# Kernel tuning notes

Measured on AMD Instinct MI355X. Metric: run time of the kernel, lower is better.

Reference implementation:

```python
import jax, jax.numpy as jnp
import numpy as np

WINDOW_SIZE = 7
C1 = 0.01 ** 2
C2 = 0.03 ** 2


def _gaussian_window(ws: int) -> jnp.ndarray:
    sigma = ws / 6.0
    coords = jnp.arange(ws, dtype=jnp.float32) - ws // 2
    g = jnp.exp(-coords ** 2 / (2 * sigma ** 2))
    g = g / g.sum()
    k3 = g[:, None, None] * g[None, :, None] * g[None, None, :]
    k3 = k3 / k3.sum()
    return k3.reshape(1, 1, ws, ws, ws)  # OIDHW


def _conv3d_same(x, w):
    pad = WINDOW_SIZE // 2
    return jax.lax.conv_general_dilated(
        x, w, window_strides=(1, 1, 1),
        padding=[(pad, pad)] * 3,
        dimension_numbers=('NCDHW', 'OIDHW', 'NCDHW'))


def setup_inputs() -> dict:
    key = jax.random.key(0)
    k1, k2 = jax.random.split(key)
    shape = (2, 1, 160, 160, 160)
    predicted = jax.random.uniform(k1, shape, dtype=jnp.float32)
    target = jax.random.uniform(k2, shape, dtype=jnp.float32)
    return {"predicted": predicted, "target": target}


def reference(predicted, target):
    window = _gaussian_window(WINDOW_SIZE)
    mu1 = _conv3d_same(predicted, window)
    mu2 = _conv3d_same(target, window)
    mu1_sq = mu1 ** 2
    mu2_sq = mu2 ** 2
    mu1_mu2 = mu1 * mu2
    sigma1_sq = _conv3d_same(predicted ** 2, window) - mu1_sq
    sigma2_sq = _conv3d_same(target ** 2, window) - mu2_sq
    sigma12 = _conv3d_same(predicted * target, window) - mu1_mu2
    ssim_map = ((2 * mu1_mu2 + C1) * (2 * sigma12 + C2)) / (
        (mu1_sq + mu2_sq + C1) * (sigma1_sq + sigma2_sq + C2))
    return 1.0 - ssim_map.mean()
```

## Files before the change

kernel.cpp:

```cpp
#include <hip/hip_runtime.h>
#include <math.h>

#define DD 160
#define HH 160
#define WW 160
#define NB 2
#define NEL (NB*DD*HH*WW)

#define XT 32
#define YT 16
#define ZC 16
#define NTHR 256
#define NZCH (DD/ZC)
#define GX (WW/XT)
#define GY (HH/YT)
#define NBLK (GX*GY*NB*NZCH)
#define NPART NBLK

#define HR 22
#define NJOB (HR*8)
#define NJOBW 44
#define CP 35

typedef float v2f __attribute__((ext_vector_type(2)));

struct G7 { float g[7]; };

__global__ __launch_bounds__(NTHR, 4) void ssim_fused(
        const float* __restrict__ p, const float* __restrict__ t,
        float* __restrict__ partial, G7 gw) {
    const int tid = threadIdx.x;
    const int tx  = tid & 31;
    const int tyo = tid >> 5;

    const int flat = blockIdx.x;
    const int w = (flat & 7) * (NBLK / 8) + (flat >> 3);
    const int bx = w % GX;
    const int by = (w / GX) % GY;
    const int bz = w / (GX * GY);

    const int x0 = bx * XT;
    const int y0 = by * YT;
    const int n  = bz / NZCH;
    const int zs = (bz % NZCH) * ZC;
    const int send = zs + ZC + 3;

    __shared__ float4 c4[2][HR][CP];

    v2f r01[2][6], r23[2][6];
#pragma unroll
    for (int yo = 0; yo < 2; ++yo)
#pragma unroll
        for (int j = 0; j < 6; ++j) {
            r01[yo][j] = (v2f)(0.f);
            r23[yo][j] = (v2f)(0.f);
        }

    const float C1v = 1e-4f, C2v = 9e-4f;
    float ssum = 0.f;
    const int hw = HH * WW;
    const float* pv = p + (size_t)n * DD * hw;
    const float* tv = t + (size_t)n * DD * hw;

    const int lane = tid & 63, wv = tid >> 6;
    const int j = wv * NJOBW + lane;
    const bool jok = lane < NJOBW;
    const int br  = j >> 3;
    const int bxg = j & 7;
    const int bgy = y0 + br - 3;
    const bool browok = jok && (unsigned)bgy < (unsigned)HH;
    const int cbase = x0 + 4 * bxg - 4;
    const int pcr = tx + (tx >> 3);
    bool qok[3];
#pragma unroll
    for (int q = 0; q < 3; ++q)
        qok[q] = browok && (unsigned)(cbase + 4 * q) < (unsigned)WW;

    const float* prow = pv + (size_t)(zs - 3) * hw + bgy * WW;
    const float* trow = tv + (size_t)(zs - 3) * hw + bgy * WW;

    float4 pfa[3], pfb[3];
    auto prefetch = [&](int sx) {
#pragma unroll
        for (int q = 0; q < 3; ++q) {
            pfa[q] = make_float4(0.f, 0.f, 0.f, 0.f);
            pfb[q] = make_float4(0.f, 0.f, 0.f, 0.f);
        }
        if (sx >= 0 && sx < DD && sx < send) {
#pragma unroll
            for (int q = 0; q < 3; ++q) {
                if (qok[q]) {
                    pfa[q] = *(const float4*)(prow + cbase + 4 * q);
                    pfb[q] = *(const float4*)(trow + cbase + 4 * q);
                }
            }
        }
    };

    auto do_B = [&](int par) {
        if (jok) {
            v2f s01[4], s23[4];
#pragma unroll
            for (int e = 0; e < 4; ++e) { s01[e] = (v2f)(0.f); s23[e] = (v2f)(0.f); }
#pragma unroll
            for (int q = 0; q < 3; ++q) {
                const float af[4] = {pfa[q].x, pfa[q].y, pfa[q].z, pfa[q].w};
                const float bf[4] = {pfb[q].x, pfb[q].y, pfb[q].z, pfb[q].w};
#pragma unroll
                for (int jj = 0; jj < 4; ++jj) {
                    const int i = 4 * q + jj;
                    v2f pt; pt[0] = af[jj]; pt[1] = bf[jj];
                    v2f ud; ud[0] = af[jj] + bf[jj]; ud[1] = af[jj] - bf[jj];
                    v2f qu = ud * ud;
#pragma unroll
                    for (int e = 0; e < 4; ++e) {
                        const int k = i - e - 1;
                        if (k >= 0 && k < 7) {
                            s01[e] = gw.g[k] * pt + s01[e];
                            s23[e] = gw.g[k] * qu + s23[e];
                        }
                    }
                }
            }
#pragma unroll
            for (int e = 0; e < 4; ++e) {
                int c = 4 * bxg + e;
                c4[par][br][c + (c >> 3)] =
                    make_float4(s01[e][0], s01[e][1], s23[e][0], s23[e][1]);
            }
        }
    };

    prefetch(zs - 3);
    do_B((zs - 3) & 1);
    prow += hw; trow += hw;
    prefetch(zs - 2);

    for (int s = zs - 3; s < send; ++s) {
        __syncthreads();

        if (s + 1 < send) do_B((s + 1) & 1);

        prow += hw; trow += hw;
        prefetch(s + 2);

        v2f m01[2], m23[2];
#pragma unroll
        for (int yo = 0; yo < 2; ++yo) {
            m01[yo] = (v2f)(0.f);
            m23[yo] = (v2f)(0.f);
        }
#pragma unroll
        for (int r8 = 0; r8 < 8; ++r8) {
            float4 v = c4[s & 1][2 * tyo + r8][pcr];
            v2f v01; v01[0] = v.x; v01[1] = v.y;
            v2f v23; v23[0] = v.z; v23[1] = v.w;
            if (r8 < 7) {
                float w2 = gw.g[r8];
                m01[0] = w2 * v01 + m01[0];
                m23[0] = w2 * v23 + m23[0];
            }
            if (r8 > 0) {
                float w2 = gw.g[r8 - 1];
                m01[1] = w2 * v01 + m01[1];
                m23[1] = w2 * v23 + m23[1];
            }
        }

#pragma unroll
        for (int yo = 0; yo < 2; ++yo) {
            v2f v01 = m01[yo], v23 = m23[yo];
            v2f cons01 = gw.g[6] * v01 + r01[yo][0];
            v2f cons23 = gw.g[6] * v23 + r23[yo][0];
#pragma unroll
            for (int jj = 0; jj < 5; ++jj) {
                r01[yo][jj] = gw.g[5 - jj] * v01 + r01[yo][jj + 1];
                r23[yo][jj] = gw.g[5 - jj] * v23 + r23[yo][jj + 1];
            }
            r01[yo][5] = gw.g[0] * v01;
            r23[yo][5] = gw.g[0] * v23;

            if (s >= zs + 3) {
                float mu1 = cons01[0], mu2 = cons01[1];
                float Eu  = cons23[0], Ew  = cons23[1];
                float mu12 = mu1 * mu2, mu1sq = mu1 * mu1, mu2sq = mu2 * mu2;
                float sumsq = 0.5f  * (Eu + Ew) - mu1sq - mu2sq;
                float s12   = 0.25f * (Eu - Ew) - mu12;
                float num = (2.f * mu12 + C1v) * (2.f * s12 + C2v);
                float den = (mu1sq + mu2sq + C1v) * (sumsq + C2v);
                ssum += num * __builtin_amdgcn_rcpf(den);
            }
        }
    }

#pragma unroll
    for (int off = 32; off > 0; off >>= 1)
        ssum += __shfl_down(ssum, off, 64);
    __shared__ float wsum[4];
    if ((tid & 63) == 0) wsum[tid >> 6] = ssum;
    __syncthreads();
    if (tid == 0)
        partial[flat] = wsum[0] + wsum[1] + wsum[2] + wsum[3];
}

__global__ __launch_bounds__(256) void ssim_final(
        const float* __restrict__ partial, float* __restrict__ out) {
    float s = 0.f;
    for (int i = threadIdx.x; i < NPART; i += 256) s += partial[i];
#pragma unroll
    for (int off = 32; off > 0; off >>= 1)
        s += __shfl_down(s, off, 64);
    __shared__ float wsum[4];
    int lane = threadIdx.x & 63, wid = threadIdx.x >> 6;
    if (lane == 0) wsum[wid] = s;
    __syncthreads();
    if (threadIdx.x == 0) {
        float tot = wsum[0] + wsum[1] + wsum[2] + wsum[3];
        out[0] = 1.0f - tot / (float)NEL;
    }
}

extern "C" void kernel_launch(void* const* d_in, const int* in_sizes, int n_in,
                              void* d_out, int out_size, void* d_ws, size_t ws_size,
                              hipStream_t stream) {
    const float* p = (const float*)d_in[0];
    const float* t = (const float*)d_in[1];
    float* out = (float*)d_out;
    float* partial = (float*)d_ws;

    G7 gw;
    {
        double s = 0.0, sig = 7.0 / 6.0;
        double g[7];
        for (int i = 0; i < 7; ++i) {
            double d = (double)i - 3.0;
            g[i] = exp(-d * d / (2.0 * sig * sig));
            s += g[i];
        }
        for (int i = 0; i < 7; ++i) gw.g[i] = (float)(g[i] / s);
    }

    ssim_fused<<<NBLK, NTHR, 0, stream>>>(p, t, partial, gw);
    ssim_final<<<1, 256, 0, stream>>>(partial, out);
}
```

Baseline: 134.9 us.

## Give each wavefront a private LDS slab to drop block-wide barriers

Each 64-lane wavefront now owns a 4-row y-strip with its own 10-row LDS region. It computes the x-convolution for its own halo rows and then reads them back, so the per-slice __syncthreads and the double-buffered shared tile go away. Each wave writes its own partial sum, which also removes the final block reduction. The cost is more redundant halo work, since 10 rows are computed per 4 output rows instead of 22 per 16. The second halo row set is loaded synchronously with no prefetch, and intra-wave LDS ordering relies on lockstep execution with no explicit wave barrier.

```diff
diff --git a/kernel.cpp b/kernel.cpp
--- a/kernel.cpp
+++ b/kernel.cpp
@@ -15,11 +15,9 @@
 #define GX (WW/XT)
 #define GY (HH/YT)
 #define NBLK (GX*GY*NB*NZCH)
-#define NPART NBLK
-
-#define HR 22
-#define NJOB (HR*8)
-#define NJOBW 44
+#define NPART (NBLK*4)
+
+#define SR 10
 #define CP 35
 
 typedef float v2f __attribute__((ext_vector_type(2)));
@@ -29,9 +27,9 @@
 __global__ __launch_bounds__(NTHR, 4) void ssim_fused(
         const float* __restrict__ p, const float* __restrict__ t,
         float* __restrict__ partial, G7 gw) {
-    const int tid = threadIdx.x;
-    const int tx  = tid & 31;
-    const int tyo = tid >> 5;
+    const int tid  = threadIdx.x;
+    const int lane = tid & 63;
+    const int wv   = tid >> 6;
 
     const int flat = blockIdx.x;
     const int w = (flat & 7) * (NBLK / 8) + (flat >> 3);
@@ -39,13 +37,14 @@
     const int by = (w / GX) % GY;
     const int bz = w / (GX * GY);
 
-    const int x0 = bx * XT;
-    const int y0 = by * YT;
-    const int n  = bz / NZCH;
-    const int zs = (bz % NZCH) * ZC;
+    const int x0  = bx * XT;
+    const int y0s = by * YT + wv * 4;
+    const int n   = bz / NZCH;
+    const int zs  = (bz % NZCH) * ZC;
     const int send = zs + ZC + 3;
 
-    __shared__ float4 c4[2][HR][CP];
+    __shared__ float4 c4s[4][SR][CP];
+    float4 (*cw)[CP] = c4s[wv];
 
     v2f r01[2][6], r23[2][6];
 #pragma unroll
@@ -62,25 +61,64 @@
     const float* pv = p + (size_t)n * DD * hw;
     const float* tv = t + (size_t)n * DD * hw;
 
-    const int lane = tid & 63, wv = tid >> 6;
-    const int j = wv * NJOBW + lane;
-    const bool jok = lane < NJOBW;
-    const int br  = j >> 3;
-    const int bxg = j & 7;
-    const int bgy = y0 + br - 3;
-    const bool browok = jok && (unsigned)bgy < (unsigned)HH;
-    const int cbase = x0 + 4 * bxg - 4;
-    const int pcr = tx + (tx >> 3);
-    bool qok[3];
-#pragma unroll
-    for (int q = 0; q < 3; ++q)
-        qok[q] = browok && (unsigned)(cbase + 4 * q) < (unsigned)WW;
-
-    const float* prow = pv + (size_t)(zs - 3) * hw + bgy * WW;
-    const float* trow = tv + (size_t)(zs - 3) * hw + bgy * WW;
+    const int xg   = lane & 7;
+    const int row1 = lane >> 3;
+    const int row2 = 8 + (lane >> 3);
+    const int gy1  = y0s + row1 - 3;
+    const int gy2  = y0s + row2 - 3;
+    const bool p2  = lane < 16;
+    const int cbase = x0 + 4 * xg - 4;
+    bool qok1[3], qok2[3];
+#pragma unroll
+    for (int q = 0; q < 3; ++q) {
+        bool cok = (unsigned)(cbase + 4 * q) < (unsigned)WW;
+        qok1[q] = cok && (unsigned)gy1 < (unsigned)HH;
+        qok2[q] = cok && (unsigned)gy2 < (unsigned)HH && p2;
+    }
+
+    const int cx  = lane & 31;
+    const int yh  = lane >> 5;
+    const int pcr = cx + (cx >> 3);
+
+    const float* pr1 = pv + (size_t)(zs - 3) * hw + gy1 * WW + cbase;
+    const float* tr1 = tv + (size_t)(zs - 3) * hw + gy1 * WW + cbase;
+    const float* pr2 = pv + (size_t)(zs - 3) * hw + gy2 * WW + cbase;
+    const float* tr2 = tv + (size_t)(zs - 3) * hw + gy2 * WW + cbase;
+
+    auto xconv = [&](const float4* A, const float4* B, int r) {
+        v2f s01[4], s23[4];
+#pragma unroll
+        for (int e = 0; e < 4; ++e) { s01[e] = (v2f)(0.f); s23[e] = (v2f)(0.f); }
+#pragma unroll
+        for (int q = 0; q < 3; ++q) {
+            const float af[4] = {A[q].x, A[q].y, A[q].z, A[q].w};
+            const float bf[4] = {B[q].x, B[q].y, B[q].z, B[q].w};
+#pragma unroll
+            for (int jj = 0; jj < 4; ++jj) {
+                const int i = 4 * q + jj;
+                v2f pt; pt[0] = af[jj]; pt[1] = bf[jj];
+                v2f ud; ud[0] = af[jj] + bf[jj]; ud[1] = af[jj] - bf[jj];
+                v2f qu = ud * ud;
+#pragma unroll
+                for (int e = 0; e < 4; ++e) {
+                    const int k = i - e - 1;
+                    if (k >= 0 && k < 7) {
+                        s01[e] = gw.g[k] * pt + s01[e];
+                        s23[e] = gw.g[k] * qu + s23[e];
+                    }
+                }
+            }
+        }
+#pragma unroll
+        for (int e = 0; e < 4; ++e) {
+            int c = 4 * xg + e;
+            cw[r][c + (c >> 3)] =
+                make_float4(s01[e][0], s01[e][1], s23[e][0], s23[e][1]);
+        }
+    };
 
     float4 pfa[3], pfb[3];
-    auto prefetch = [&](int sx) {
+    auto prefetch1 = [&](int sx) {
 #pragma unroll
         for (int q = 0; q < 3; ++q) {
             pfa[q] = make_float4(0.f, 0.f, 0.f, 0.f);
@@ -89,60 +127,39 @@
         if (sx >= 0 && sx < DD && sx < send) {
 #pragma unroll
             for (int q = 0; q < 3; ++q) {
-                if (qok[q]) {
-                    pfa[q] = *(const float4*)(prow + cbase + 4 * q);
-                    pfb[q] = *(const float4*)(trow + cbase + 4 * q);
+                if (qok1[q]) {
+                    pfa[q] = *(const float4*)(pr1 + 4 * q);
+                    pfb[q] = *(const float4*)(tr1 + 4 * q);
                 }
             }
         }
     };
 
-    auto do_B = [&](int par) {
-        if (jok) {
-            v2f s01[4], s23[4];
-#pragma unroll
-            for (int e = 0; e < 4; ++e) { s01[e] = (v2f)(0.f); s23[e] = (v2f)(0.f); }
-#pragma unroll
-            for (int q = 0; q < 3; ++q) {
-                const float af[4] = {pfa[q].x, pfa[q].y, pfa[q].z, pfa[q].w};
-                const float bf[4] = {pfb[q].x, pfb[q].y, pfb[q].z, pfb[q].w};
-#pragma unroll
-                for (int jj = 0; jj < 4; ++jj) {
-                    const int i = 4 * q + jj;
-                    v2f pt; pt[0] = af[jj]; pt[1] = bf[jj];
-                    v2f ud; ud[0] = af[jj] + bf[jj]; ud[1] = af[jj] - bf[jj];
-                    v2f qu = ud * ud;
-#pragma unroll
-                    for (int e = 0; e < 4; ++e) {
-                        const int k = i - e - 1;
-                        if (k >= 0 && k < 7) {
-                            s01[e] = gw.g[k] * pt + s01[e];
-                            s23[e] = gw.g[k] * qu + s23[e];
-                        }
+    prefetch1(zs - 3);
+
+    for (int s = zs - 3; s < send; ++s) {
+        const bool valid = (s >= 0) && (s < DD);
+
+        if (valid) {
+            xconv(pfa, pfb, row1);
+            if (p2) {
+                float4 a2[3], b2[3];
+#pragma unroll
+                for (int q = 0; q < 3; ++q) {
+                    a2[q] = make_float4(0.f, 0.f, 0.f, 0.f);
+                    b2[q] = make_float4(0.f, 0.f, 0.f, 0.f);
+                    if (qok2[q]) {
+                        a2[q] = *(const float4*)(pr2 + 4 * q);
+                        b2[q] = *(const float4*)(tr2 + 4 * q);
                     }
                 }
-            }
-#pragma unroll
-            for (int e = 0; e < 4; ++e) {
-                int c = 4 * bxg + e;
-                c4[par][br][c + (c >> 3)] =
-                    make_float4(s01[e][0], s01[e][1], s23[e][0], s23[e][1]);
-            }
-        }
-    };
-
-    prefetch(zs - 3);
-    do_B((zs - 3) & 1);
-    prow += hw; trow += hw;
-    prefetch(zs - 2);
-
-    for (int s = zs - 3; s < send; ++s) {
-        __syncthreads();
-
-        if (s + 1 < send) do_B((s + 1) & 1);
-
-        prow += hw; trow += hw;
-        prefetch(s + 2);
+                xconv(a2, b2, row2);
+            }
+        }
+
+        pr1 += hw; tr1 += hw;
+        prefetch1(s + 1);
+        pr2 += hw; tr2 += hw;
 
         v2f m01[2], m23[2];
 #pragma unroll
@@ -150,20 +167,22 @@
             m01[yo] = (v2f)(0.f);
             m23[yo] = (v2f)(0.f);
         }
-#pragma unroll
-        for (int r8 = 0; r8 < 8; ++r8) {
-            float4 v = c4[s & 1][2 * tyo + r8][pcr];
-            v2f v01; v01[0] = v.x; v01[1] = v.y;
-            v2f v23; v23[0] = v.z; v23[1] = v.w;
-            if (r8 < 7) {
-                float w2 = gw.g[r8];
-                m01[0] = w2 * v01 + m01[0];
-                m23[0] = w2 * v23 + m23[0];
-            }
-            if (r8 > 0) {
-                float w2 = gw.g[r8 - 1];
-                m01[1] = w2 * v01 + m01[1];
-                m23[1] = w2 * v23 + m23[1];
+        if (valid) {
+#pragma unroll
+            for (int r8 = 0; r8 < 8; ++r8) {
+                float4 v = cw[2 * yh + r8][pcr];
+                v2f v01; v01[0] = v.x; v01[1] = v.y;
+                v2f v23; v23[0] = v.z; v23[1] = v.w;
+                if (r8 < 7) {
+                    float w2 = gw.g[r8];
+                    m01[0] = w2 * v01 + m01[0];
+                    m23[0] = w2 * v23 + m23[0];
+                }
+                if (r8 > 0) {
+                    float w2 = gw.g[r8 - 1];
+                    m01[1] = w2 * v01 + m01[1];
+                    m23[1] = w2 * v23 + m23[1];
+                }
             }
         }
 
@@ -196,11 +215,8 @@
 #pragma unroll
     for (int off = 32; off > 0; off >>= 1)
         ssum += __shfl_down(ssum, off, 64);
-    __shared__ float wsum[4];
-    if ((tid & 63) == 0) wsum[tid >> 6] = ssum;
-    __syncthreads();
-    if (tid == 0)
-        partial[flat] = wsum[0] + wsum[1] + wsum[2] + wsum[3];
+    if (lane == 0)
+        partial[flat * 4 + wv] = ssum;
 }
 
 __global__ __launch_bounds__(256) void ssim_final(
```

Measured after the change: 163.9 us. 1.22x slower.
